# Kernel optimization log

Hardware: AMD Instinct MI355X
Metric: run time of the kernel (lower is better)

Reference implementation:

```python
import jax, jax.numpy as jnp
import numpy as np

T = 20000          # document length in tokens
EMBED_DIM = 300    # GloVe 840B.300d
STATE_DIM = 400    # 2 * lstm_dim (bidirectional)
HIDDEN = 150       # Scorer hidden_dim default
MAX_N = 10         # span widths 1..10
G_DIM = 2 * STATE_DIM + EMBED_DIM  # 1100


def _mlp3(x, W1, b1, W2, b2, W3, b3):
    # Scorer: Linear -> ReLU -> Linear -> ReLU -> Linear(->1)
    h = jax.nn.relu(x @ W1 + b1)
    h = jax.nn.relu(h @ W2 + b2)
    return h @ W3 + b3


def _span_features(embeds, states, attn_logits):
    """Vectorized SpanEncoder: for every window of width n in 1..MAX_N,
    softmax the per-token attention logits within the window, attention-pool
    the word embeddings, and concat [state_start, state_end, pooled].
    Returns g of shape [sum_n (T-n+1), G_DIM]."""
    gs = []
    for n in range(1, MAX_N + 1):
        S = T - n + 1  # number of width-n spans
        # [n, S] windowed logits and [n, S, E] windowed embeds via shifted slices
        a = jnp.stack([attn_logits[j:j + S] for j in range(n)], axis=0)
        w = jax.nn.softmax(a, axis=0)  # softmax within each span (dim=0 in torch)
        we = jnp.stack([embeds[j:j + S] for j in range(n)], axis=0)
        pooled = jnp.einsum('ns,nse->se', w, we)  # [S, E]
        g = jnp.concatenate([states[:S], states[n - 1:n - 1 + S], pooled], axis=-1)
        gs.append(g)
    return jnp.concatenate(gs, axis=0)


def setup_inputs() -> dict:
    key = jax.random.key(0)
    ks = jax.random.split(key, 16)
    sc = 0.05
    return {
        'embeds': jax.random.normal(ks[0], (T, EMBED_DIM), jnp.float32),
        'states': jax.random.normal(ks[1], (T, STATE_DIM), jnp.float32),
        'attn_W1': jax.random.normal(ks[2], (STATE_DIM, HIDDEN), jnp.float32) * sc,
        'attn_b1': jnp.zeros((HIDDEN,), jnp.float32),
        'attn_W2': jax.random.normal(ks[3], (HIDDEN, HIDDEN), jnp.float32) * sc,
        'attn_b2': jnp.zeros((HIDDEN,), jnp.float32),
        'attn_W3': jax.random.normal(ks[4], (HIDDEN, 1), jnp.float32) * sc,
        'attn_b3': jnp.zeros((1,), jnp.float32),
        'sc_W1': jax.random.normal(ks[5], (G_DIM, HIDDEN), jnp.float32) * sc,
        'sc_b1': jnp.zeros((HIDDEN,), jnp.float32),
        'sc_W2': jax.random.normal(ks[6], (HIDDEN, HIDDEN), jnp.float32) * sc,
        'sc_b2': jnp.zeros((HIDDEN,), jnp.float32),
        'sc_W3': jax.random.normal(ks[7], (HIDDEN, 1), jnp.float32) * sc,
        'sc_b3': jnp.zeros((1,), jnp.float32),
    }


def reference(embeds, states, attn_W1, attn_b1, attn_W2, attn_b2, attn_W3, attn_b3,
              sc_W1, sc_b1, sc_W2, sc_b2, sc_W3, sc_b3):
    # SpanAttention: per-token scalar attention logit from the BiLSTM state
    attn_logits = _mlp3(states, attn_W1, attn_b1, attn_W2, attn_b2, attn_W3, attn_b3)[:, 0]
    # SpanEncoder: ragged windowed attention pooling + boundary-state concat
    g = _span_features(embeds, states, attn_logits)  # [10T-45, 1100]
    # SpanScorer: MLP score per span
    scores = _mlp3(g, sc_W1, sc_b1, sc_W2, sc_b2, sc_W3, sc_b3)[:, 0]
    return scores
```

## Files before the change

### kernel.cpp

```cpp
#include <hip/hip_runtime.h>
#include <hip/hip_bf16.h>
#include <math.h>

#define T_LEN 20000
#define HID 150

typedef __attribute__((ext_vector_type(8))) __bf16 bf16x8;
typedef __attribute__((ext_vector_type(4))) float f32x4;

__device__ __forceinline__ short f2bf(float f) {
    unsigned u = __float_as_uint(f);
    u = (u + 0x7fff + ((u >> 16) & 1)) >> 16;
    return (short)u;
}

__device__ __forceinline__ unsigned pk2(float a, float b) {
    __hip_bfloat162 h = __float22bfloat162_rn(make_float2(a, b));
    return *(unsigned*)&h;
}

__device__ __forceinline__ bf16x8 cvt8(float4 a, float4 b) {
    union { unsigned u[4]; bf16x8 v; } r;
    r.u[0] = pk2(a.x, a.y);
    r.u[1] = pk2(a.z, a.w);
    r.u[2] = pk2(b.x, b.y);
    r.u[3] = pk2(b.z, b.w);
    return r.v;
}

__device__ __forceinline__ float2 ubf2(unsigned u) {
    return make_float2(__uint_as_float(u << 16),
                       __uint_as_float(u & 0xffff0000u));
}

__global__ __launch_bounds__(256) void wprep(
    const float* __restrict__ sc_W1, const float* __restrict__ attn_W1,
    const float* __restrict__ attn_W2, const float* __restrict__ sc_W2,
    short* __restrict__ frag)
{
    int t = blockIdx.x * 256 + threadIdx.x;
    if (t >= 302080) return;
    float v = 0.f;
    if (t < 199680) {
        int e = t & 7, g = t >> 3;
        int lane = g & 63, h = g >> 6;
        int ks = h % 13, nt = h / 13;
        int k = ks * 32 + (lane >> 4) * 8 + e;
        int cs = (nt % 10) * 16 + (lane & 15);
        if (k < 400 && cs < HID) {
            if (nt < 10)      v = sc_W1[(long)k * HID + cs];
            else if (nt < 20) v = sc_W1[(long)(400 + k) * HID + cs];
            else              v = attn_W1[(long)k * HID + cs];
        }
    } else if (t < 250880) {
        int r = t - 199680;
        int e = r & 7, g = r >> 3;
        int lane = g & 63, h = g >> 6;
        int ks = h % 10, nt = h / 10;
        int k = ks * 32 + (lane >> 4) * 8 + e;
        int cs = nt * 16 + (lane & 15);
        if (k < 300 && cs < HID) v = sc_W1[(long)(800 + k) * HID + cs];
    } else if (t < 276480) {
        int r = t - 250880;
        int e = r & 7, g = r >> 3;
        int lane = g & 63, h = g >> 6;
        int ks = h % 5, nt = h / 5;
        int k = ks * 32 + (lane >> 4) * 8 + e;
        int cs = nt * 16 + (lane & 15);
        if (k < HID && cs < HID) v = attn_W2[(long)k * HID + cs];
    } else {
        int r = t - 276480;
        int e = r & 7, g = r >> 3;
        int lane = g & 63, h = g >> 6;
        int ks = h % 5, nt = h / 5;
        int k = ks * 32 + (lane >> 4) * 8 + e;
        int cs = nt * 16 + (lane & 15);
        if (k < HID && cs < HID) v = sc_W2[(long)k * HID + cs];
    }
    frag[t] = f2bf(v);
}

__global__ __launch_bounds__(256) void fusedAP(
    const float* __restrict__ states, const float* __restrict__ embeds,
    const short* __restrict__ frag,
    const float* __restrict__ scb1, const float* __restrict__ ab1,
    const float* __restrict__ ab2, const float* __restrict__ aW3,
    const float* __restrict__ ab3,
    short* __restrict__ Ubf, short* __restrict__ Vbf, short* __restrict__ Pbf,
    float* __restrict__ logits)
{
    __shared__ short h1s[16 * 168];
    __shared__ float red[16][4];
    __shared__ float sb1[160], ab1s[160];
    const int tid = threadIdx.x;
    const int w = tid >> 6, lane = tid & 63;
    const int ml = lane & 15, kg = lane >> 4;
    const int m0 = blockIdx.x * 16;

    for (int t = tid; t < 160; t += 256) {
        sb1[t]  = (t < HID) ? scb1[t] : 0.f;
        ab1s[t] = (t < HID) ? ab1[t]  : 0.f;
    }
    __syncthreads();

    const float* Arow = states + (long)(m0 + ml) * 400;
    const int nT = (w < 2) ? 8 : 7;

    f32x4 acc[8];
    #pragma unroll
    for (int t = 0; t < 8; ++t) acc[t] = (f32x4){0.f, 0.f, 0.f, 0.f};

    #pragma unroll
    for (int ks = 0; ks < 13; ++ks) {
        int k = ks * 32 + kg * 8;
        float4 a0 = make_float4(0.f, 0.f, 0.f, 0.f);
        float4 a1 = make_float4(0.f, 0.f, 0.f, 0.f);
        if (k + 4 <= 400) a0 = *(const float4*)&Arow[k];
        if (k + 8 <= 400) a1 = *(const float4*)&Arow[k + 4];
        bf16x8 af = cvt8(a0, a1);
        #pragma unroll
        for (int t = 0; t < 8; ++t) {
            if (t < nT) {
                int nt = 4 * t + w;
                bf16x8 bf = *(const bf16x8*)&frag[(long)(((nt * 13 + ks) << 6) | lane) << 3];
                acc[t] = __builtin_amdgcn_mfma_f32_16x16x32_bf16(bf, af, acc[t], 0, 0, 0);
            }
        }
    }

    #pragma unroll
    for (int t = 0; t < 8; ++t) {
        if (t < nT) {
            int nt = 4 * t + w;
            if (nt < 10) {
                int col0 = nt * 16 + kg * 4;
                float v[4];
                #pragma unroll
                for (int r = 0; r < 4; ++r) {
                    int c = col0 + r;
                    v[r] = (c < HID) ? acc[t][r] + sb1[c] : 0.f;
                }
                *(uint2*)&Ubf[(long)(m0 + ml) * 160 + col0] =
                    make_uint2(pk2(v[0], v[1]), pk2(v[2], v[3]));
            } else if (nt < 20) {
                int col0 = (nt - 10) * 16 + kg * 4;
                float v[4];
                #pragma unroll
                for (int r = 0; r < 4; ++r) {
                    int c = col0 + r;
                    v[r] = (c < HID) ? acc[t][r] : 0.f;
                }
                *(uint2*)&Vbf[(long)(m0 + ml) * 160 + col0] =
                    make_uint2(pk2(v[0], v[1]), pk2(v[2], v[3]));
            } else {
                int col0 = (nt - 20) * 16 + kg * 4;
                float v[4];
                #pragma unroll
                for (int r = 0; r < 4; ++r) {
                    int c = col0 + r;
                    v[r] = (c < HID) ? fmaxf(acc[t][r] + ab1s[c], 0.f) : 0.f;
                }
                *(uint2*)&h1s[ml * 168 + col0] =
                    make_uint2(pk2(v[0], v[1]), pk2(v[2], v[3]));
            }
        }
    }
    __syncthreads();

    {
        const short* fP = frag + 199680;
        const float* Erow = embeds + (long)(m0 + ml) * 300;
        const int nTp = (w < 2) ? 3 : 2;
        f32x4 accP[3];
        #pragma unroll
        for (int t = 0; t < 3; ++t) accP[t] = (f32x4){0.f, 0.f, 0.f, 0.f};

        #pragma unroll
        for (int ks = 0; ks < 10; ++ks) {
            int k = ks * 32 + kg * 8;
            float4 a0 = make_float4(0.f, 0.f, 0.f, 0.f);
            float4 a1 = make_float4(0.f, 0.f, 0.f, 0.f);
            if (k + 4 <= 300) a0 = *(const float4*)&Erow[k];
            if (k + 8 <= 300) a1 = *(const float4*)&Erow[k + 4];
            bf16x8 af = cvt8(a0, a1);
            #pragma unroll
            for (int t = 0; t < 3; ++t) {
                if (t < nTp) {
                    int nt = 4 * t + w;
                    bf16x8 bf = *(const bf16x8*)&fP[(long)(((nt * 10 + ks) << 6) | lane) << 3];
                    accP[t] = __builtin_amdgcn_mfma_f32_16x16x32_bf16(bf, af, accP[t], 0, 0, 0);
                }
            }
        }

        #pragma unroll
        for (int t = 0; t < 3; ++t) {
            if (t < nTp) {
                int nt = 4 * t + w;
                int col0 = nt * 16 + kg * 4;
                float v[4];
                #pragma unroll
                for (int r = 0; r < 4; ++r) {
                    int c = col0 + r;
                    v[r] = (c < HID) ? accP[t][r] : 0.f;
                }
                *(uint2*)&Pbf[(long)(m0 + ml) * 160 + col0] =
                    make_uint2(pk2(v[0], v[1]), pk2(v[2], v[3]));
            }
        }
    }

    const short* fAt2 = frag + 250880;
    bf16x8 af2[5];
    #pragma unroll
    for (int ks = 0; ks < 5; ++ks)
        af2[ks] = *(const bf16x8*)&h1s[ml * 168 + ks * 32 + kg * 8];

    const int nT2 = (w < 2) ? 3 : 2;
    float score[4] = {0.f, 0.f, 0.f, 0.f};
    #pragma unroll
    for (int t = 0; t < 3; ++t) {
        if (t < nT2) {
            int nt = 4 * t + w;
            f32x4 a2 = {0.f, 0.f, 0.f, 0.f};
            #pragma unroll
            for (int ks = 0; ks < 5; ++ks) {
                bf16x8 bf = *(const bf16x8*)&fAt2[(long)(((nt * 5 + ks) << 6) | lane) << 3];
                a2 = __builtin_amdgcn_mfma_f32_16x16x32_bf16(af2[ks], bf, a2, 0, 0, 0);
            }
            int col = nt * 16 + ml;
            float b2v = (col < HID) ? ab2[col] : 0.f;
            float w3v = (col < HID) ? aW3[col] : 0.f;
            #pragma unroll
            for (int r = 0; r < 4; ++r)
                score[r] += fmaxf(a2[r] + b2v, 0.f) * w3v;
        }
    }
    #pragma unroll
    for (int r = 0; r < 4; ++r) {
        score[r] += __shfl_xor(score[r], 1);
        score[r] += __shfl_xor(score[r], 2);
        score[r] += __shfl_xor(score[r], 4);
        score[r] += __shfl_xor(score[r], 8);
    }
    if (ml == 0) {
        #pragma unroll
        for (int r = 0; r < 4; ++r) red[kg * 4 + r][w] = score[r];
    }
    __syncthreads();
    if (tid < 16)
        logits[m0 + tid] = red[tid][0] + red[tid][1] + red[tid][2] + red[tid][3] + ab3[0];
}

__global__ __launch_bounds__(256) void span_all(
    const short* __restrict__ Ubf, const short* __restrict__ Vbf,
    const short* __restrict__ Pbf, const float* __restrict__ logits,
    const short* __restrict__ fW2, const float* __restrict__ b2,
    const float* __restrict__ W3, const float* __restrict__ b3,
    float* __restrict__ out)
{
    __shared__ short h1s[2][32 * 168];
    __shared__ float red[2][32][2];
    __shared__ float Ls[48], ebuf[48];
    __shared__ float b2s[160], W3s[160];

    const int tid = threadIdx.x;
    const int s0 = blockIdx.x * 32;
    const int nlo = blockIdx.y ? 6 : 1;
    const int nhi = blockIdx.y ? 10 : 5;

    if (tid < 48) {
        int r = s0 + tid; if (r > T_LEN - 1) r = T_LEN - 1;
        Ls[tid] = (tid < 41) ? logits[r] : -1e30f;
    }
    for (int t = tid; t < 160; t += 256) {
        b2s[t] = (t < HID) ? b2[t] : 0.f;
        W3s[t] = (t < HID) ? W3[t] : 0.f;
    }
    __syncthreads();
    if (tid < 48) {
        float M = -1e30f;
        for (int t = 0; t < 41; ++t) M = fmaxf(M, Ls[t]);
        ebuf[tid] = (tid < 41) ? expf(Ls[tid] - M) : 0.f;
    }
    __syncthreads();

    const int i = tid >> 3;
    const int q = tid & 7;
    const int d0 = 20 * q;
    const int s = s0 + i;
    int su = s; if (su > T_LEN - 1) su = T_LEN - 1;

    float Ur[20];
    {
        const uint2* U2 = (const uint2*)&Ubf[(long)su * 160 + d0];
        #pragma unroll
        for (int c = 0; c < 5; ++c) {
            uint2 uv = U2[c];
            float2 a = ubf2(uv.x), b_ = ubf2(uv.y);
            Ur[4 * c + 0] = a.x;  Ur[4 * c + 1] = a.y;
            Ur[4 * c + 2] = b_.x; Ur[4 * c + 3] = b_.y;
        }
    }
    float accp[20];
    #pragma unroll
    for (int d = 0; d < 20; ++d) accp[d] = 0.f;
    float den = 0.f;

    for (int j = 0; j < nlo - 1; ++j) {
        int rr_ = s + j; if (rr_ > T_LEN - 1) rr_ = T_LEN - 1;
        float e = ebuf[i + j];
        den += e;
        const uint2* P2 = (const uint2*)&Pbf[(long)rr_ * 160 + d0];
        #pragma unroll
        for (int c = 0; c < 5; ++c) {
            uint2 pv = P2[c];
            float2 a = ubf2(pv.x), b_ = ubf2(pv.y);
            accp[4 * c + 0] += e * a.x;  accp[4 * c + 1] += e * a.y;
            accp[4 * c + 2] += e * b_.x; accp[4 * c + 3] += e * b_.y;
        }
    }

    const int w = tid >> 6, lane = tid & 63;
    const int ml = lane & 15, kg = lane >> 4;
    const int mt = w >> 1;
    const int nt0 = (w & 1) * 5;
    const float bb = b3[0];

    auto phase1 = [&](int n, int p) {
        int rr_ = s + n - 1; if (rr_ > T_LEN - 1) rr_ = T_LEN - 1;
        float e = ebuf[i + n - 1];
        den += e;
        {
            const uint2* P2 = (const uint2*)&Pbf[(long)rr_ * 160 + d0];
            #pragma unroll
            for (int c = 0; c < 5; ++c) {
                uint2 pv = P2[c];
                float2 a = ubf2(pv.x), b_ = ubf2(pv.y);
                accp[4 * c + 0] += e * a.x;  accp[4 * c + 1] += e * a.y;
                accp[4 * c + 2] += e * b_.x; accp[4 * c + 3] += e * b_.y;
            }
        }
        float invd = 1.f / den;
        {
            const uint2* V2 = (const uint2*)&Vbf[(long)rr_ * 160 + d0];
            #pragma unroll
            for (int c = 0; c < 5; ++c) {
                uint2 vv = V2[c];
                float2 a = ubf2(vv.x), b_ = ubf2(vv.y);
                float x0 = fmaxf(Ur[4 * c + 0] + a.x  + accp[4 * c + 0] * invd, 0.f);
                float x1 = fmaxf(Ur[4 * c + 1] + a.y  + accp[4 * c + 1] * invd, 0.f);
                float x2 = fmaxf(Ur[4 * c + 2] + b_.x + accp[4 * c + 2] * invd, 0.f);
                float x3 = fmaxf(Ur[4 * c + 3] + b_.y + accp[4 * c + 3] * invd, 0.f);
                *(uint2*)&h1s[p][i * 168 + d0 + 4 * c] =
                    make_uint2(pk2(x0, x1), pk2(x2, x3));
            }
        }
    };

    phase1(nlo, 0);
    __syncthreads();

    for (int n = nlo; n <= nhi; ++n) {
        const int p = (n - nlo) & 1;
        if (n < nhi) phase1(n + 1, 1 - p);

        bf16x8 af[5];
        #pragma unroll
        for (int ks = 0; ks < 5; ++ks)
            af[ks] = *(const bf16x8*)&h1s[p][(mt * 16 + ml) * 168 + ks * 32 + kg * 8];

        float sc[4] = {0.f, 0.f, 0.f, 0.f};
        #pragma unroll
        for (int j = 0; j < 5; ++j) {
            int nt = nt0 + j;
            f32x4 a2 = {0.f, 0.f, 0.f, 0.f};
            #pragma unroll
            for (int ks = 0; ks < 5; ++ks) {
                bf16x8 bf = *(const bf16x8*)&fW2[(long)(((nt * 5 + ks) << 6) | lane) << 3];
                a2 = __builtin_amdgcn_mfma_f32_16x16x32_bf16(af[ks], bf, a2, 0, 0, 0);
            }
            int col = nt * 16 + ml;
            float b2v = b2s[col], w3v = W3s[col];
            #pragma unroll
            for (int r = 0; r < 4; ++r)
                sc[r] += fmaxf(a2[r] + b2v, 0.f) * w3v;
        }
        #pragma unroll
        for (int r = 0; r < 4; ++r) {
            sc[r] += __shfl_xor(sc[r], 1);
            sc[r] += __shfl_xor(sc[r], 2);
            sc[r] += __shfl_xor(sc[r], 4);
            sc[r] += __shfl_xor(sc[r], 8);
        }
        if (ml == 0) {
            #pragma unroll
            for (int r = 0; r < 4; ++r)
                red[p][mt * 16 + kg * 4 + r][w & 1] = sc[r];
        }
        __syncthreads();
        if (tid < 32) {
            int S = T_LEN - n + 1;
            int off = (n - 1) * (T_LEN + 1) - (n - 1) * n / 2;
            int sr = s0 + tid;
            if (sr < S) out[off + sr] = red[p][tid][0] + red[p][tid][1] + bb;
        }
    }
}

extern "C" void kernel_launch(void* const* d_in, const int* in_sizes, int n_in,
                              void* d_out, int out_size, void* d_ws, size_t ws_size,
                              hipStream_t stream) {
    const float* embeds  = (const float*)d_in[0];
    const float* states  = (const float*)d_in[1];
    const float* attn_W1 = (const float*)d_in[2];
    const float* attn_b1 = (const float*)d_in[3];
    const float* attn_W2 = (const float*)d_in[4];
    const float* attn_b2 = (const float*)d_in[5];
    const float* attn_W3 = (const float*)d_in[6];
    const float* attn_b3 = (const float*)d_in[7];
    const float* sc_W1   = (const float*)d_in[8];
    const float* sc_b1   = (const float*)d_in[9];
    const float* sc_W2   = (const float*)d_in[10];
    const float* sc_b2   = (const float*)d_in[11];
    const float* sc_W3   = (const float*)d_in[12];
    const float* sc_b3   = (const float*)d_in[13];
    float* out = (float*)d_out;

    short* wsS = (short*)d_ws;
    short* Ubf = wsS;
    short* Vbf = wsS + 3200256;
    short* Pbf = wsS + 6400512;
    short* frag = wsS + 9600768;
    float* logits = (float*)(wsS + 9902848);

    wprep<<<1180, 256, 0, stream>>>(sc_W1, attn_W1, attn_W2, sc_W2, frag);
    fusedAP<<<1250, 256, 0, stream>>>(states, embeds, frag, sc_b1, attn_b1,
                                      attn_b2, attn_W3, attn_b3,
                                      Ubf, Vbf, Pbf, logits);
    span_all<<<dim3(625, 2), 256, 0, stream>>>(Ubf, Vbf, Pbf, logits,
                                               frag + 276480, sc_b2, sc_W3, sc_b3,
                                               out);
}
```

Baseline: 194.7 us.

## Stage bf16 A tiles in LDS and software-pipeline weight fragment loads

In the first kernel, the states and embeds rows are converted to bf16 once and staged in shared memory in MFMA fragment layout, and all B fragments for a k-step are loaded before the MFMAs are issued. Launch bounds now request 4 blocks per SM. In the span scorer loop, the W2 fragments for the next tile are prefetched into registers while the current tile's MFMAs run. Phase1 for the next width is moved after the A-fragment reads. The aim is to hide global load latency behind MFMA work, at the cost of extra registers and LDS, which could lower occupancy or cause spills.

```diff
diff --git a/kernel.cpp b/kernel.cpp
--- a/kernel.cpp
+++ b/kernel.cpp
@@ -80,7 +80,26 @@
     frag[t] = f2bf(v);
 }
 
-__global__ __launch_bounds__(256) void fusedAP(
+template<int NT, int KS>
+__device__ __forceinline__ void mm_tiles(
+    const short* __restrict__ fb,
+    const short* As,
+    int w, int lane, f32x4* acc)
+{
+    #pragma unroll
+    for (int ks = 0; ks < KS; ++ks) {
+        bf16x8 af = *(const bf16x8*)&As[(ks * 64 + lane) * 8];
+        bf16x8 bfr[NT];
+        #pragma unroll
+        for (int t = 0; t < NT; ++t)
+            bfr[t] = *(const bf16x8*)&fb[((4 * t + w) * KS + ks) << 9];
+        #pragma unroll
+        for (int t = 0; t < NT; ++t)
+            acc[t] = __builtin_amdgcn_mfma_f32_16x16x32_bf16(bfr[t], af, acc[t], 0, 0, 0);
+    }
+}
+
+__global__ __launch_bounds__(256, 4) void fusedAP(
     const float* __restrict__ states, const float* __restrict__ embeds,
     const short* __restrict__ frag,
     const float* __restrict__ scb1, const float* __restrict__ ab1,
@@ -89,6 +108,7 @@
     short* __restrict__ Ubf, short* __restrict__ Vbf, short* __restrict__ Pbf,
     float* __restrict__ logits)
 {
+    __shared__ short As[13 * 64 * 8];
     __shared__ short h1s[16 * 168];
     __shared__ float red[16][4];
     __shared__ float sb1[160], ab1s[160];
@@ -101,33 +121,25 @@
         sb1[t]  = (t < HID) ? scb1[t] : 0.f;
         ab1s[t] = (t < HID) ? ab1[t]  : 0.f;
     }
-    __syncthreads();
-
-    const float* Arow = states + (long)(m0 + ml) * 400;
+    for (int g = tid; g < 13 * 64; g += 256) {
+        int ks = g >> 6, l2 = g & 63;
+        int k = ks * 32 + ((l2 >> 4) << 3);
+        const float* Ar = states + (long)(m0 + (l2 & 15)) * 400;
+        float4 a0 = make_float4(0.f, 0.f, 0.f, 0.f), a1 = a0;
+        if (k + 4 <= 400) a0 = *(const float4*)&Ar[k];
+        if (k + 8 <= 400) a1 = *(const float4*)&Ar[k + 4];
+        *(bf16x8*)&As[g * 8] = cvt8(a0, a1);
+    }
+    __syncthreads();
+
+    f32x4 acc[8];
+    #pragma unroll
+    for (int t = 0; t < 8; ++t) acc[t] = (f32x4){0.f, 0.f, 0.f, 0.f};
+    const short* fb = frag + lane * 8;
+    if (w < 2) mm_tiles<8, 13>(fb, As, w, lane, acc);
+    else       mm_tiles<7, 13>(fb, As, w, lane, acc);
+
     const int nT = (w < 2) ? 8 : 7;
-
-    f32x4 acc[8];
-    #pragma unroll
-    for (int t = 0; t < 8; ++t) acc[t] = (f32x4){0.f, 0.f, 0.f, 0.f};
-
-    #pragma unroll
-    for (int ks = 0; ks < 13; ++ks) {
-        int k = ks * 32 + kg * 8;
-        float4 a0 = make_float4(0.f, 0.f, 0.f, 0.f);
-        float4 a1 = make_float4(0.f, 0.f, 0.f, 0.f);
-        if (k + 4 <= 400) a0 = *(const float4*)&Arow[k];
-        if (k + 8 <= 400) a1 = *(const float4*)&Arow[k + 4];
-        bf16x8 af = cvt8(a0, a1);
-        #pragma unroll
-        for (int t = 0; t < 8; ++t) {
-            if (t < nT) {
-                int nt = 4 * t + w;
-                bf16x8 bf = *(const bf16x8*)&frag[(long)(((nt * 13 + ks) << 6) | lane) << 3];
-                acc[t] = __builtin_amdgcn_mfma_f32_16x16x32_bf16(bf, af, acc[t], 0, 0, 0);
-            }
-        }
-    }
-
     #pragma unroll
     for (int t = 0; t < 8; ++t) {
         if (t < nT) {
@@ -167,32 +179,26 @@
     }
     __syncthreads();
 
+    for (int g = tid; g < 10 * 64; g += 256) {
+        int ks = g >> 6, l2 = g & 63;
+        int k = ks * 32 + ((l2 >> 4) << 3);
+        const float* Er = embeds + (long)(m0 + (l2 & 15)) * 300;
+        float4 a0 = make_float4(0.f, 0.f, 0.f, 0.f), a1 = a0;
+        if (k + 4 <= 300) a0 = *(const float4*)&Er[k];
+        if (k + 8 <= 300) a1 = *(const float4*)&Er[k + 4];
+        *(bf16x8*)&As[g * 8] = cvt8(a0, a1);
+    }
+    __syncthreads();
+
     {
-        const short* fP = frag + 199680;
-        const float* Erow = embeds + (long)(m0 + ml) * 300;
+        f32x4 accP[3];
+        #pragma unroll
+        for (int t = 0; t < 3; ++t) accP[t] = (f32x4){0.f, 0.f, 0.f, 0.f};
+        const short* fP = frag + 199680 + lane * 8;
+        if (w < 2) mm_tiles<3, 10>(fP, As, w, lane, accP);
+        else       mm_tiles<2, 10>(fP, As, w, lane, accP);
+
         const int nTp = (w < 2) ? 3 : 2;
-        f32x4 accP[3];
-        #pragma unroll
-        for (int t = 0; t < 3; ++t) accP[t] = (f32x4){0.f, 0.f, 0.f, 0.f};
-
-        #pragma unroll
-        for (int ks = 0; ks < 10; ++ks) {
-            int k = ks * 32 + kg * 8;
-            float4 a0 = make_float4(0.f, 0.f, 0.f, 0.f);
-            float4 a1 = make_float4(0.f, 0.f, 0.f, 0.f);
-            if (k + 4 <= 300) a0 = *(const float4*)&Erow[k];
-            if (k + 8 <= 300) a1 = *(const float4*)&Erow[k + 4];
-            bf16x8 af = cvt8(a0, a1);
-            #pragma unroll
-            for (int t = 0; t < 3; ++t) {
-                if (t < nTp) {
-                    int nt = 4 * t + w;
-                    bf16x8 bf = *(const bf16x8*)&fP[(long)(((nt * 10 + ks) << 6) | lane) << 3];
-                    accP[t] = __builtin_amdgcn_mfma_f32_16x16x32_bf16(bf, af, accP[t], 0, 0, 0);
-                }
-            }
-        }
-
         #pragma unroll
         for (int t = 0; t < 3; ++t) {
             if (t < nTp) {
@@ -210,7 +216,7 @@
         }
     }
 
-    const short* fAt2 = frag + 250880;
+    const short* fAt2 = frag + 250880 + lane * 8;
     bf16x8 af2[5];
     #pragma unroll
     for (int ks = 0; ks < 5; ++ks)
@@ -222,12 +228,14 @@
     for (int t = 0; t < 3; ++t) {
         if (t < nT2) {
             int nt = 4 * t + w;
+            bf16x8 wb[5];
+            #pragma unroll
+            for (int ks = 0; ks < 5; ++ks)
+                wb[ks] = *(const bf16x8*)&fAt2[(nt * 5 + ks) << 9];
             f32x4 a2 = {0.f, 0.f, 0.f, 0.f};
             #pragma unroll
-            for (int ks = 0; ks < 5; ++ks) {
-                bf16x8 bf = *(const bf16x8*)&fAt2[(long)(((nt * 5 + ks) << 6) | lane) << 3];
-                a2 = __builtin_amdgcn_mfma_f32_16x16x32_bf16(af2[ks], bf, a2, 0, 0, 0);
-            }
+            for (int ks = 0; ks < 5; ++ks)
+                a2 = __builtin_amdgcn_mfma_f32_16x16x32_bf16(af2[ks], wb[ks], a2, 0, 0, 0);
             int col = nt * 16 + ml;
             float b2v = (col < HID) ? ab2[col] : 0.f;
             float w3v = (col < HID) ? aW3[col] : 0.f;
@@ -326,6 +334,7 @@
     const int mt = w >> 1;
     const int nt0 = (w & 1) * 5;
     const float bb = b3[0];
+    const short* fw = fW2 + ((nt0 * 5) << 9) + lane * 8;
 
     auto phase1 = [&](int n, int p) {
         int rr_ = s + n - 1; if (rr_ > T_LEN - 1) rr_ = T_LEN - 1;
@@ -363,28 +372,38 @@
 
     for (int n = nlo; n <= nhi; ++n) {
         const int p = (n - nlo) & 1;
-        if (n < nhi) phase1(n + 1, 1 - p);
 
         bf16x8 af[5];
         #pragma unroll
         for (int ks = 0; ks < 5; ++ks)
             af[ks] = *(const bf16x8*)&h1s[p][(mt * 16 + ml) * 168 + ks * 32 + kg * 8];
 
+        if (n < nhi) phase1(n + 1, 1 - p);
+
+        bf16x8 wc[5], wn[5];
+        #pragma unroll
+        for (int ks = 0; ks < 5; ++ks)
+            wc[ks] = *(const bf16x8*)&fw[ks << 9];
+
         float sc[4] = {0.f, 0.f, 0.f, 0.f};
         #pragma unroll
         for (int j = 0; j < 5; ++j) {
-            int nt = nt0 + j;
+            if (j < 4) {
+                #pragma unroll
+                for (int ks = 0; ks < 5; ++ks)
+                    wn[ks] = *(const bf16x8*)&fw[((j + 1) * 5 + ks) << 9];
+            }
             f32x4 a2 = {0.f, 0.f, 0.f, 0.f};
             #pragma unroll
-            for (int ks = 0; ks < 5; ++ks) {
-                bf16x8 bf = *(const bf16x8*)&fW2[(long)(((nt * 5 + ks) << 6) | lane) << 3];
-                a2 = __builtin_amdgcn_mfma_f32_16x16x32_bf16(af[ks], bf, a2, 0, 0, 0);
-            }
-            int col = nt * 16 + ml;
+            for (int ks = 0; ks < 5; ++ks)
+                a2 = __builtin_amdgcn_mfma_f32_16x16x32_bf16(af[ks], wc[ks], a2, 0, 0, 0);
+            int col = (nt0 + j) * 16 + ml;
             float b2v = b2s[col], w3v = W3s[col];
             #pragma unroll
             for (int r = 0; r < 4; ++r)
                 sc[r] += fmaxf(a2[r] + b2v, 0.f) * w3v;
+            #pragma unroll
+            for (int ks = 0; ks < 5; ++ks) wc[ks] = wn[ks];
         }
         #pragma unroll
         for (int r = 0; r < 4; ++r) {
```

New measurement: 191.6 us. No clear change (-1.6%).
